# Kernel optimization log

Hardware: AMD Instinct MI355X
Metric: run time of the kernel (lower is better)

Reference implementation:

```python
import jax, jax.numpy as jnp
import numpy as np

N_HEADS = 16
D_HEAD = 64
THETA = 10000.0


def _rope_tables(S, dh, dtype):
    inv_freq = 1.0 / (THETA ** (jnp.arange(0, dh, 2, dtype=jnp.float32) / dh))  # [dh/2]
    ang = jnp.arange(S, dtype=jnp.float32)[:, None] * inv_freq[None, :]  # [S, dh/2]
    return jnp.cos(ang).astype(dtype), jnp.sin(ang).astype(dtype)


def _apply_rope(t, cos, sin):
    # t: [B,S,H,dh]; interleaved complex pairs (even=real, odd=imag)
    B, S, H, dh = t.shape
    tr = t.reshape(B, S, H, dh // 2, 2)
    a, b = tr[..., 0], tr[..., 1]
    c = cos[None, :, None, :]
    s = sin[None, :, None, :]
    ra = a * c - b * s
    rb = a * s + b * c
    return jnp.stack([ra, rb], axis=-1).reshape(B, S, H, dh)


def setup_inputs() -> dict:
    key = jax.random.key(0)
    ks = jax.random.split(key, 5)
    B, S, D = 2, 2048, 1024
    x = jax.random.normal(ks[0], (B, S, D), dtype=jnp.float32)
    scale = 1.0 / np.sqrt(D)
    wq = jax.random.normal(ks[1], (D, D), dtype=jnp.float32) * scale
    wk = jax.random.normal(ks[2], (D, D), dtype=jnp.float32) * scale
    wv = jax.random.normal(ks[3], (D, D), dtype=jnp.float32) * scale
    wo = jax.random.normal(ks[4], (D, D), dtype=jnp.float32) * scale
    return {"x": x, "wq": wq, "wk": wk, "wv": wv, "wo": wo}


def reference(x, wq, wk, wv, wo):
    B, S, D = x.shape
    H, dh = N_HEADS, D_HEAD
    q = (x @ wq).reshape(B, S, H, dh)
    k = (x @ wk).reshape(B, S, H, dh)
    v = (x @ wv).reshape(B, S, H, dh)
    cos, sin = _rope_tables(S, dh, x.dtype)
    q = _apply_rope(q, cos, sin)
    k = _apply_rope(k, cos, sin)
    # [B,H,S,S] scores
    scale = 1.0 / np.sqrt(dh).astype(np.float32)
    attn = jnp.einsum('bqhd,bkhd->bhqk', q, k) * scale
    causal = jnp.tril(jnp.ones((S, S), dtype=bool))[None, None]
    attn = jnp.where(causal, attn, -jnp.inf)
    probs = jax.nn.softmax(attn, axis=-1)
    head_out = jnp.einsum('bhqk,bkhd->bqhd', probs, v).reshape(B, S, D)
    return head_out @ wo
```

## Files before the change

### kernel.cpp

```cpp
#include <hip/hip_runtime.h>
#include <hip/hip_bf16.h>

#define S_LEN   2048
#define BATCH   2
#define NH      16
#define DH      64
#define DMODEL  1024
#define MTOT    (BATCH * S_LEN)

typedef __attribute__((ext_vector_type(4))) float f32x4;
typedef __attribute__((ext_vector_type(8))) short s16x8;
typedef __attribute__((ext_vector_type(4))) short s16x4;

#define MFMA_BF16(a, b, c) __builtin_amdgcn_mfma_f32_16x16x32_bf16((a), (b), (c), 0, 0, 0)

static __device__ __forceinline__ short f2bf(float f) {
    union { float f; unsigned u; } v; v.f = f;
    unsigned r = v.u + 0x7fffu + ((v.u >> 16) & 1u);
    return (short)(r >> 16);
}

static __device__ __forceinline__ unsigned cvtpk_bf16(float lo, float hi) {
    unsigned r;
    asm volatile("v_cvt_pk_bf16_f32 %0, %1, %2" : "=v"(r) : "v"(lo), "v"(hi));
    return r;
}

static __device__ __forceinline__ void gload_lds16(const void* g, void* l) {
    __builtin_amdgcn_global_load_lds(
        (const __attribute__((address_space(1))) void*)g,
        (__attribute__((address_space(3))) void*)l, 16, 0, 0);
}

#define VM_WAIT(N) asm volatile("s_waitcnt vmcnt(" #N ")" ::: "memory")

static __device__ __forceinline__ void barrier_sync() {
    asm volatile("" ::: "memory");
    __builtin_amdgcn_s_barrier();
    asm volatile("" ::: "memory");
}

__global__ __launch_bounds__(256) void prep_all(const float* __restrict__ wq,
                                                const float* __restrict__ wk,
                                                const float* __restrict__ wv,
                                                const float* __restrict__ wo,
                                                const float* __restrict__ x,
                                                short* __restrict__ wtb,
                                                short* __restrict__ xb,
                                                float* __restrict__ cosT,
                                                float* __restrict__ sinT) {
    const int t = threadIdx.x;
    if (blockIdx.z < 4) {
        const float* W = (blockIdx.z == 0) ? wq : (blockIdx.z == 1) ? wk
                       : (blockIdx.z == 2) ? wv : wo;
        short* out = wtb + (size_t)blockIdx.z * DMODEL * DMODEL;

        __shared__ short T[64][72];
        const int k0 = blockIdx.y * 64, n0 = blockIdx.x * 64;

        #pragma unroll
        for (int p = 0; p < 4; ++p) {
            const int kk = p * 16 + (t >> 4);
            const int nn = (t & 15) * 4;
            f32x4 v = *(const f32x4*)(W + (size_t)(k0 + kk) * DMODEL + n0 + nn);
            #pragma unroll
            for (int j = 0; j < 4; ++j) T[nn + j][kk] = f2bf(v[j]);
        }
        __syncthreads();
        #pragma unroll
        for (int p = 0; p < 4; ++p) {
            const int nn = p * 16 + (t >> 4);
            const int kk = (t & 15) * 4;
            *(s16x4*)(out + (size_t)(n0 + nn) * DMODEL + k0 + kk) = *(const s16x4*)&T[nn][kk];
        }
    } else {
        const int blk = blockIdx.y * 16 + blockIdx.x;
        #pragma unroll
        for (int jj = 0; jj < 8; ++jj) {
            const size_t i = ((size_t)jj * 65536 + blk * 256 + t) * 8;
            f32x4 a = *(const f32x4*)(x + i);
            f32x4 b = *(const f32x4*)(x + i + 4);
            s16x8 o;
            #pragma unroll
            for (int j = 0; j < 4; ++j) { o[j] = f2bf(a[j]); o[4 + j] = f2bf(b[j]); }
            *(s16x8*)(xb + i) = o;
        }
        const int idx = blk * 256 + t;
        const int s = idx >> 5, ii = idx & 31;
        const float inv = exp2f(-(float)ii * (13.287712379549449f / 32.0f));
        const float ang = (float)s * inv;
        cosT[idx] = cosf(ang);
        sinT[idx] = sinf(ang);
    }
}

__device__ __forceinline__ void gemm_tile(const short* __restrict__ A,
                                          const short* __restrict__ Bt,
                                          int m0, int n0, short* SM,
                                          f32x4 acc[4][4]) {
    const int tid  = threadIdx.x;
    const int lane = tid & 63;
    const int wv   = tid >> 6;
    const int wm   = (wv >> 1) * 64;
    const int wn   = (wv & 1) * 64;
    const int g = lane >> 4, c16 = lane & 15;

    short* Asb = SM;
    short* Bsb = SM + 12288;

    const int srow = tid >> 2;
    const int schk = (tid & 3) ^ ((tid >> 3) & 3);
    const short* ga0 = A  + (size_t)(m0 + srow)      * DMODEL + schk * 8;
    const short* ga1 = A  + (size_t)(m0 + 64 + srow) * DMODEL + schk * 8;
    const short* gb0 = Bt + (size_t)(n0 + srow)      * DMODEL + schk * 8;
    const short* gb1 = Bt + (size_t)(n0 + 64 + srow) * DMODEL + schk * 8;
    const int lw = wv * 512;

    #define STAGE_G(buf, ko) do { \
        gload_lds16(ga0 + (ko), Asb + (buf) * 4096 + lw); \
        gload_lds16(ga1 + (ko), Asb + (buf) * 4096 + 2048 + lw); \
        gload_lds16(gb0 + (ko), Bsb + (buf) * 4096 + lw); \
        gload_lds16(gb1 + (ko), Bsb + (buf) * 4096 + 2048 + lw); \
    } while (0)

    STAGE_G(0, 0);
    STAGE_G(1, 32);

    const int rlo = (g ^ ((c16 >> 1) & 3)) << 3;
    for (int ks = 0; ks < 32; ++ks) {
        if (ks < 31) { VM_WAIT(4); } else { VM_WAIT(0); }
        barrier_sync();
        if (ks + 2 < 32) STAGE_G((ks + 2) % 3, (ks + 2) * 32);
        const int cur = ks % 3;
        s16x8 af[4], bfr[4];
        #pragma unroll
        for (int i = 0; i < 4; ++i)
            af[i] = *(const s16x8*)&Asb[cur * 4096 + (wm + i * 16 + c16) * 32 + rlo];
        #pragma unroll
        for (int j = 0; j < 4; ++j)
            bfr[j] = *(const s16x8*)&Bsb[cur * 4096 + (wn + j * 16 + c16) * 32 + rlo];
        #pragma unroll
        for (int i = 0; i < 4; ++i)
            #pragma unroll
            for (int j = 0; j < 4; ++j)
                acc[i][j] = MFMA_BF16(af[i], bfr[j], acc[i][j]);
    }
    #undef STAGE_G
}

__global__ __launch_bounds__(256) void gemm_qkv(const short* __restrict__ xb,
                                                const short* __restrict__ wtb,
                                                short* __restrict__ Qo,
                                                short* __restrict__ Ko,
                                                short* __restrict__ Vt,
                                                const float* __restrict__ cosT,
                                                const float* __restrict__ sinT) {
    __shared__ __align__(16) short SM[24576];

    const int dd    = blockIdx.x + 24 * blockIdx.y;
    const int xcd   = dd & 7;
    const int local = dd >> 3;
    const int ty = (xcd & 3) * 8 + local / 12;
    const int tx = (xcd >> 2) * 12 + local % 12;
    const int m0 = ty * 128, n0 = tx * 128;
    const int z  = tx >> 3;

    f32x4 acc[4][4] = {};
    gemm_tile(xb, wtb, m0, n0, SM, acc);

    const int tid  = threadIdx.x;
    const int lane = tid & 63;
    const int wv   = tid >> 6;
    const int wm   = (wv >> 1) * 64, wn = (wv & 1) * 64;
    const int g = lane >> 4, c16 = lane & 15;
    const int hbase = (n0 & 1023) >> 6;

    barrier_sync();
    short (*RP)[136] = (short(*)[136])SM;

    if (z < 2) {
        short* outp = (z == 0) ? Qo : Ko;
        const float post = (z == 0) ? 0.18033688011112042f : 1.0f;
        #pragma unroll
        for (int j = 0; j < 4; ++j) {
            const int nl = wn + j * 16 + c16;
            const int d  = (n0 + nl) & 63;
            #pragma unroll
            for (int i = 0; i < 4; ++i) {
                #pragma unroll
                for (int r = 0; r < 4; ++r) {
                    const int ml = wm + i * 16 + g * 4 + r;
                    const int s  = (m0 + ml) & (S_LEN - 1);
                    float v = acc[i][j][r];
                    float vo = __shfl_xor(v, 1, 64);
                    float cs = cosT[s * 32 + (d >> 1)];
                    float sn = sinT[s * 32 + (d >> 1)];
                    float res = (d & 1) ? (vo * sn + v * cs) : (v * cs - vo * sn);
                    RP[ml][nl] = f2bf(res * post);
                }
            }
        }
        barrier_sync();
        #pragma unroll
        for (int pass = 0; pass < 8; ++pass) {
            const int row = pass * 32 + (tid >> 3);
            const int k   = tid & 7;
            const int hh = row >> 7, ss = row & 127;
            const int m = m0 + ss;
            const int s = m & (S_LEN - 1), b = m >> 11;
            short* dst = outp + (((size_t)b * NH + hbase + hh) * S_LEN + s) * DH + k * 8;
            *(s16x8*)dst = *(const s16x8*)&RP[ss][hh * 64 + k * 8];
        }
    } else {
        #pragma unroll
        for (int j = 0; j < 4; ++j) {
            const int nl = wn + j * 16 + c16;
            #pragma unroll
            for (int i = 0; i < 4; ++i) {
                const int mlb = wm + i * 16 + g * 4;
                s16x4 pk;
                #pragma unroll
                for (int r = 0; r < 4; ++r) pk[r] = f2bf(acc[i][j][r]);
                *(s16x4*)&RP[nl][mlb] = pk;
            }
        }
        barrier_sync();
        const int b = m0 >> 11, sr0 = m0 & (S_LEN - 1);
        #pragma unroll
        for (int pass = 0; pass < 8; ++pass) {
            const int row = pass * 16 + (tid >> 4);
            const int k   = tid & 15;
            const int h = hbase + (row >> 6), d = row & 63;
            short* dst = Vt + (((size_t)b * NH + h) * DH + d) * S_LEN + sr0 + k * 8;
            *(s16x8*)dst = *(const s16x8*)&RP[row][k * 8];
        }
    }
}

__global__ __launch_bounds__(256) void attn(const short* __restrict__ Q,
                                            const short* __restrict__ K,
                                            const short* __restrict__ Vt,
                                            short* __restrict__ O) {
    const int tid  = threadIdx.x;
    const int lane = tid & 63;
    const int w    = tid >> 6;
    const int g = lane >> 4, c16 = lane & 15;
    const int bid  = blockIdx.x + 16 * blockIdx.y;
    const int cxcd = bid & 7, jj = bid >> 3;
    const int bh   = (jj & 3) * 8 + cxcd;
    const int bx   = jj >> 2;
    const size_t base = (size_t)bh * S_LEN * DH;
    const short* Kb = K + base;
    const short* Vb = Vt + (size_t)bh * DH * S_LEN;
    const int b = bh >> 4, h = bh & 15;

    __shared__ __align__(16) short KL[3][4096];
    __shared__ __align__(16) short VL[3][4096];
    __shared__ __align__(16) short P2[4][16][72];

    const int kr = tid >> 3;
    const int kc = (tid & 7) ^ (kr & 7);
    const short* kg0 = Kb + (size_t)kr * DH + (kc << 3);
    const short* kg1 = Kb + (size_t)(32 + kr) * DH + (kc << 3);
    const short* vg0 = Vb + (size_t)kr * S_LEN + (kc << 3);
    const short* vg1 = Vb + (size_t)(32 + kr) * S_LEN + (kc << 3);
    const int lw = w * 512;
    const int kx = c16 & 7;

    #pragma unroll 1
    for (int half = 0; half < 2; ++half) {
        const int ci = half ? bx : 31 - bx;
        const int ntiles = ci + 1;
        const int wq0 = ci * 64 + w * 16;

        gload_lds16(kg0, &KL[0][lw]);
        gload_lds16(kg1, &KL[0][2048 + lw]);
        gload_lds16(vg0, &VL[0][lw]);
        gload_lds16(vg1, &VL[0][2048 + lw]);
        s16x8 bq0 = *(const s16x8*)(Q + base + (size_t)(wq0 + c16) * DH + g * 8);
        s16x8 bq1 = *(const s16x8*)(Q + base + (size_t)(wq0 + c16) * DH + 32 + g * 8);
        if (ntiles > 1) {
            gload_lds16(kg0 + (size_t)64 * DH, &KL[1][lw]);
            gload_lds16(kg1 + (size_t)64 * DH, &KL[1][2048 + lw]);
            gload_lds16(vg0 + 64, &VL[1][lw]);
            gload_lds16(vg1 + 64, &VL[1][2048 + lw]);
        }

        f32x4 o[4] = {};
        float lsum = 0.f;

        for (int tt = 0; tt < ntiles; ++tt) {
            if (tt + 1 < ntiles) { VM_WAIT(4); } else { VM_WAIT(0); }
            barrier_sync();
            if (tt + 2 < ntiles) {
                const int nb = (tt + 2) % 3;
                const size_t ko = (size_t)(tt + 2) * 64;
                gload_lds16(kg0 + ko * DH, &KL[nb][lw]);
                gload_lds16(kg1 + ko * DH, &KL[nb][2048 + lw]);
                gload_lds16(vg0 + ko,      &VL[nb][lw]);
                gload_lds16(vg1 + ko,      &VL[nb][2048 + lw]);
            }
            const int cur = tt % 3;

            f32x4 s[4];
            __builtin_amdgcn_s_setprio(1);
            #pragma unroll
            for (int cg = 0; cg < 4; ++cg) {
                const int krow = (cg * 16 + c16) * 64;
                s16x8 kf0 = *(const s16x8*)&KL[cur][krow + ((g ^ kx) << 3)];
                s16x8 kf1 = *(const s16x8*)&KL[cur][krow + (((4 + g) ^ kx) << 3)];
                f32x4 zz = {};
                zz = MFMA_BF16(kf0, bq0, zz);
                s[cg] = MFMA_BF16(kf1, bq1, zz);
            }
            __builtin_amdgcn_s_setprio(0);

            s16x8 vf[4][2];
            #pragma unroll
            for (int nt = 0; nt < 4; ++nt) {
                const int vr = (nt * 16 + c16) * 64;
                vf[nt][0] = *(const s16x8*)&VL[cur][vr + ((g ^ kx) << 3)];
                vf[nt][1] = *(const s16x8*)&VL[cur][vr + (((4 + g) ^ kx) << 3)];
            }

            const bool diag = (tt == ci);
            const int qrel = w * 16 + c16;
            #pragma unroll
            for (int cg = 0; cg < 4; ++cg) {
                float e[4];
                #pragma unroll
                for (int r = 0; r < 4; ++r) {
                    e[r] = exp2f(s[cg][r]);
                    if (diag && (cg * 16 + g * 4 + r > qrel)) e[r] = 0.f;
                }
                lsum += (e[0] + e[1]) + (e[2] + e[3]);
                uint2 pk;
                pk.x = cvtpk_bf16(e[0], e[1]);
                pk.y = cvtpk_bf16(e[2], e[3]);
                *(uint2*)&P2[w][c16][cg * 16 + g * 4] = pk;
            }
            asm volatile("s_waitcnt lgkmcnt(0)" ::: "memory");
            __builtin_amdgcn_sched_barrier(0);
            s16x8 ap0 = *(const s16x8*)&P2[w][c16][g * 8];
            s16x8 ap1 = *(const s16x8*)&P2[w][c16][32 + g * 8];

            __builtin_amdgcn_s_setprio(1);
            #pragma unroll
            for (int nt = 0; nt < 4; ++nt) {
                o[nt] = MFMA_BF16(ap0, vf[nt][0], o[nt]);
                o[nt] = MFMA_BF16(ap1, vf[nt][1], o[nt]);
            }
            __builtin_amdgcn_s_setprio(0);
        }

        float lt = lsum;
        lt += __shfl_xor(lt, 16, 64);
        lt += __shfl_xor(lt, 32, 64);
        #pragma unroll
        for (int r = 0; r < 4; ++r) {
            const float linv = 1.0f / __shfl(lt, g * 4 + r, 64);
            #pragma unroll
            for (int nt = 0; nt < 4; ++nt) {
                O[((size_t)(b * S_LEN + wq0 + g * 4 + r)) * DMODEL
                  + h * DH + nt * 16 + c16] = f2bf(o[nt][r] * linv);
            }
        }
    }
}

__global__ __launch_bounds__(256) void gemm_o(const short* __restrict__ Ob,
                                              const short* __restrict__ WoT,
                                              float* __restrict__ C) {
    __shared__ __align__(16) short SMl[24576];

    const int dd = blockIdx.x + 8 * blockIdx.y;
    const int ti = (dd & 7) * 32 + (dd >> 3);
    const int tx = ti & 7, ty = ti >> 3;
    const int m0 = ty * 128, n0 = tx * 128;

    f32x4 acc[4][4] = {};
    gemm_tile(Ob, WoT, m0, n0, SMl, acc);

    const int tid  = threadIdx.x;
    const int lane = tid & 63;
    const int wv   = tid >> 6;
    const int wm   = (wv >> 1) * 64, wn = (wv & 1) * 64;
    const int g = lane >> 4, c16 = lane & 15;

    #pragma unroll
    for (int i = 0; i < 4; ++i)
        #pragma unroll
        for (int j = 0; j < 4; ++j) {
            const int n = n0 + wn + j * 16 + c16;
            #pragma unroll
            for (int r = 0; r < 4; ++r) {
                const int m = m0 + wm + i * 16 + g * 4 + r;
                C[(size_t)m * DMODEL + n] = acc[i][j][r];
            }
        }
}

extern "C" void kernel_launch(void* const* d_in, const int* in_sizes, int n_in,
                              void* d_out, int out_size, void* d_ws, size_t ws_size,
                              hipStream_t stream) {
    const float* x  = (const float*)d_in[0];
    const float* wq = (const float*)d_in[1];
    const float* wk = (const float*)d_in[2];
    const float* wv = (const float*)d_in[3];
    const float* wo = (const float*)d_in[4];
    float* out = (float*)d_out;

    char* ws = (char*)d_ws;
    short* wtb  = (short*)ws;
    short* xb   = (short*)(ws + (8ull  << 20));
    float* cosT = (float*)(ws + (16ull << 20));
    float* sinT = (float*)(ws + (16ull << 20) + (256ull << 10));
    short* Qb   = (short*)(ws + (17ull << 20));
    short* Kb   = (short*)(ws + (25ull << 20));
    short* Vtb  = (short*)(ws + (33ull << 20));
    short* Ob   = (short*)(ws + (41ull << 20));

    prep_all<<<dim3(16, 16, 5), 256, 0, stream>>>(wq, wk, wv, wo, x,
                                                  wtb, xb, cosT, sinT);

    gemm_qkv<<<dim3(24, 32), 256, 0, stream>>>(xb, wtb, Qb, Kb, Vtb, cosT, sinT);
    attn    <<<dim3(16, 32), 256, 0, stream>>>(Qb, Kb, Vtb, Ob);
    gemm_o  <<<dim3(8, 32),  256, 0, stream>>>(Ob, wtb + 3ull * DMODEL * DMODEL, out);
}
```

Baseline: 110.0 us.

## Split attention blocks per query tile and use 128x64 tiles for output GEMM

The attention kernel drops the paired causal work balancing, where one block handled two query tiles, and now launches one block per (batch-head, query tile), for twice as many blocks. The K/V ring shrinks from triple to double buffering with a barrier at the end of each iteration. The output projection moves to a new 128x64 tile routine with more blocks, so more of the GPU's compute units get work. The cost is uneven per-block work under the causal mask, shallower prefetch in attention, and more redundant A-tile loads in the output GEMM.

```diff
diff --git a/kernel.cpp b/kernel.cpp
--- a/kernel.cpp
+++ b/kernel.cpp
@@ -148,6 +148,58 @@
     #undef STAGE_G
 }
 
+__device__ __forceinline__ void gemm_tile64(const short* __restrict__ A,
+                                            const short* __restrict__ Bt,
+                                            int m0, int n0, short* SM,
+                                            f32x4 acc[4][2]) {
+    const int tid  = threadIdx.x;
+    const int lane = tid & 63;
+    const int wv   = tid >> 6;
+    const int wm   = (wv >> 1) * 64;
+    const int wn   = (wv & 1) * 32;
+    const int g = lane >> 4, c16 = lane & 15;
+
+    short* Asb = SM;
+    short* Bsb = SM + 12288;
+
+    const int srow = tid >> 2;
+    const int schk = (tid & 3) ^ ((tid >> 3) & 3);
+    const short* ga0 = A  + (size_t)(m0 + srow)      * DMODEL + schk * 8;
+    const short* ga1 = A  + (size_t)(m0 + 64 + srow) * DMODEL + schk * 8;
+    const short* gb0 = Bt + (size_t)(n0 + srow)      * DMODEL + schk * 8;
+    const int lw = wv * 512;
+
+    #define SG64(buf, ko) do { \
+        gload_lds16(ga0 + (ko), Asb + (buf) * 4096 + lw); \
+        gload_lds16(ga1 + (ko), Asb + (buf) * 4096 + 2048 + lw); \
+        gload_lds16(gb0 + (ko), Bsb + (buf) * 2048 + lw); \
+    } while (0)
+
+    SG64(0, 0);
+    SG64(1, 32);
+
+    const int rlo = (g ^ ((c16 >> 1) & 3)) << 3;
+    for (int ks = 0; ks < 32; ++ks) {
+        if (ks < 31) { VM_WAIT(3); } else { VM_WAIT(0); }
+        barrier_sync();
+        if (ks + 2 < 32) SG64((ks + 2) % 3, (ks + 2) * 32);
+        const int cur = ks % 3;
+        s16x8 af[4], bfr[2];
+        #pragma unroll
+        for (int i = 0; i < 4; ++i)
+            af[i] = *(const s16x8*)&Asb[cur * 4096 + (wm + i * 16 + c16) * 32 + rlo];
+        #pragma unroll
+        for (int j = 0; j < 2; ++j)
+            bfr[j] = *(const s16x8*)&Bsb[cur * 2048 + (wn + j * 16 + c16) * 32 + rlo];
+        #pragma unroll
+        for (int i = 0; i < 4; ++i)
+            #pragma unroll
+            for (int j = 0; j < 2; ++j)
+                acc[i][j] = MFMA_BF16(af[i], bfr[j], acc[i][j]);
+    }
+    #undef SG64
+}
+
 __global__ __launch_bounds__(256) void gemm_qkv(const short* __restrict__ xb,
                                                 const short* __restrict__ wtb,
                                                 short* __restrict__ Qo,
@@ -245,17 +297,17 @@
     const int lane = tid & 63;
     const int w    = tid >> 6;
     const int g = lane >> 4, c16 = lane & 15;
-    const int bid  = blockIdx.x + 16 * blockIdx.y;
-    const int cxcd = bid & 7, jj = bid >> 3;
-    const int bh   = (jj & 3) * 8 + cxcd;
-    const int bx   = jj >> 2;
+    const int bh = blockIdx.x;
+    const int ci = 31 - blockIdx.y;
+    const int ntiles = ci + 1;
+    const int wq0 = ci * 64 + w * 16;
     const size_t base = (size_t)bh * S_LEN * DH;
     const short* Kb = K + base;
     const short* Vb = Vt + (size_t)bh * DH * S_LEN;
     const int b = bh >> 4, h = bh & 15;
 
-    __shared__ __align__(16) short KL[3][4096];
-    __shared__ __align__(16) short VL[3][4096];
+    __shared__ __align__(16) short KL[2][4096];
+    __shared__ __align__(16) short VL[2][4096];
     __shared__ __align__(16) short P2[4][16][72];
 
     const int kr = tid >> 3;
@@ -267,103 +319,93 @@
     const int lw = w * 512;
     const int kx = c16 & 7;
 
-    #pragma unroll 1
-    for (int half = 0; half < 2; ++half) {
-        const int ci = half ? bx : 31 - bx;
-        const int ntiles = ci + 1;
-        const int wq0 = ci * 64 + w * 16;
-
-        gload_lds16(kg0, &KL[0][lw]);
-        gload_lds16(kg1, &KL[0][2048 + lw]);
-        gload_lds16(vg0, &VL[0][lw]);
-        gload_lds16(vg1, &VL[0][2048 + lw]);
-        s16x8 bq0 = *(const s16x8*)(Q + base + (size_t)(wq0 + c16) * DH + g * 8);
-        s16x8 bq1 = *(const s16x8*)(Q + base + (size_t)(wq0 + c16) * DH + 32 + g * 8);
-        if (ntiles > 1) {
-            gload_lds16(kg0 + (size_t)64 * DH, &KL[1][lw]);
-            gload_lds16(kg1 + (size_t)64 * DH, &KL[1][2048 + lw]);
-            gload_lds16(vg0 + 64, &VL[1][lw]);
-            gload_lds16(vg1 + 64, &VL[1][2048 + lw]);
-        }
-
-        f32x4 o[4] = {};
-        float lsum = 0.f;
-
-        for (int tt = 0; tt < ntiles; ++tt) {
-            if (tt + 1 < ntiles) { VM_WAIT(4); } else { VM_WAIT(0); }
-            barrier_sync();
-            if (tt + 2 < ntiles) {
-                const int nb = (tt + 2) % 3;
-                const size_t ko = (size_t)(tt + 2) * 64;
-                gload_lds16(kg0 + ko * DH, &KL[nb][lw]);
-                gload_lds16(kg1 + ko * DH, &KL[nb][2048 + lw]);
-                gload_lds16(vg0 + ko,      &VL[nb][lw]);
-                gload_lds16(vg1 + ko,      &VL[nb][2048 + lw]);
+    gload_lds16(kg0, &KL[0][lw]);
+    gload_lds16(kg1, &KL[0][2048 + lw]);
+    gload_lds16(vg0, &VL[0][lw]);
+    gload_lds16(vg1, &VL[0][2048 + lw]);
+    s16x8 bq0 = *(const s16x8*)(Q + base + (size_t)(wq0 + c16) * DH + g * 8);
+    s16x8 bq1 = *(const s16x8*)(Q + base + (size_t)(wq0 + c16) * DH + 32 + g * 8);
+    VM_WAIT(0);
+    barrier_sync();
+
+    f32x4 o[4] = {};
+    float lsum = 0.f;
+
+    for (int tt = 0; tt < ntiles; ++tt) {
+        const int cur = tt & 1;
+        const bool more = (tt + 1 < ntiles);
+        if (more) {
+            const size_t ko = (size_t)(tt + 1) * 64;
+            gload_lds16(kg0 + ko * DH, &KL[cur ^ 1][lw]);
+            gload_lds16(kg1 + ko * DH, &KL[cur ^ 1][2048 + lw]);
+            gload_lds16(vg0 + ko,      &VL[cur ^ 1][lw]);
+            gload_lds16(vg1 + ko,      &VL[cur ^ 1][2048 + lw]);
+        }
+
+        f32x4 s[4];
+        __builtin_amdgcn_s_setprio(1);
+        #pragma unroll
+        for (int cg = 0; cg < 4; ++cg) {
+            const int krow = (cg * 16 + c16) * 64;
+            s16x8 kf0 = *(const s16x8*)&KL[cur][krow + ((g ^ kx) << 3)];
+            s16x8 kf1 = *(const s16x8*)&KL[cur][krow + (((4 + g) ^ kx) << 3)];
+            f32x4 zz = {};
+            zz = MFMA_BF16(kf0, bq0, zz);
+            s[cg] = MFMA_BF16(kf1, bq1, zz);
+        }
+        __builtin_amdgcn_s_setprio(0);
+
+        s16x8 vf[4][2];
+        #pragma unroll
+        for (int nt = 0; nt < 4; ++nt) {
+            const int vr = (nt * 16 + c16) * 64;
+            vf[nt][0] = *(const s16x8*)&VL[cur][vr + ((g ^ kx) << 3)];
+            vf[nt][1] = *(const s16x8*)&VL[cur][vr + (((4 + g) ^ kx) << 3)];
+        }
+
+        const bool diag = (tt == ci);
+        const int qrel = w * 16 + c16;
+        #pragma unroll
+        for (int cg = 0; cg < 4; ++cg) {
+            float e[4];
+            #pragma unroll
+            for (int r = 0; r < 4; ++r) {
+                e[r] = exp2f(s[cg][r]);
+                if (diag && (cg * 16 + g * 4 + r > qrel)) e[r] = 0.f;
             }
-            const int cur = tt % 3;
-
-            f32x4 s[4];
-            __builtin_amdgcn_s_setprio(1);
-            #pragma unroll
-            for (int cg = 0; cg < 4; ++cg) {
-                const int krow = (cg * 16 + c16) * 64;
-                s16x8 kf0 = *(const s16x8*)&KL[cur][krow + ((g ^ kx) << 3)];
-                s16x8 kf1 = *(const s16x8*)&KL[cur][krow + (((4 + g) ^ kx) << 3)];
-                f32x4 zz = {};
-                zz = MFMA_BF16(kf0, bq0, zz);
-                s[cg] = MFMA_BF16(kf1, bq1, zz);
-            }
-            __builtin_amdgcn_s_setprio(0);
-
-            s16x8 vf[4][2];
-            #pragma unroll
-            for (int nt = 0; nt < 4; ++nt) {
-                const int vr = (nt * 16 + c16) * 64;
-                vf[nt][0] = *(const s16x8*)&VL[cur][vr + ((g ^ kx) << 3)];
-                vf[nt][1] = *(const s16x8*)&VL[cur][vr + (((4 + g) ^ kx) << 3)];
-            }
-
-            const bool diag = (tt == ci);
-            const int qrel = w * 16 + c16;
-            #pragma unroll
-            for (int cg = 0; cg < 4; ++cg) {
-                float e[4];
-                #pragma unroll
-                for (int r = 0; r < 4; ++r) {
-                    e[r] = exp2f(s[cg][r]);
-                    if (diag && (cg * 16 + g * 4 + r > qrel)) e[r] = 0.f;
-                }
-                lsum += (e[0] + e[1]) + (e[2] + e[3]);
-                uint2 pk;
-                pk.x = cvtpk_bf16(e[0], e[1]);
-                pk.y = cvtpk_bf16(e[2], e[3]);
-                *(uint2*)&P2[w][c16][cg * 16 + g * 4] = pk;
-            }
-            asm volatile("s_waitcnt lgkmcnt(0)" ::: "memory");
-            __builtin_amdgcn_sched_barrier(0);
-            s16x8 ap0 = *(const s16x8*)&P2[w][c16][g * 8];
-            s16x8 ap1 = *(const s16x8*)&P2[w][c16][32 + g * 8];
-
-            __builtin_amdgcn_s_setprio(1);
-            #pragma unroll
-            for (int nt = 0; nt < 4; ++nt) {
-                o[nt] = MFMA_BF16(ap0, vf[nt][0], o[nt]);
-                o[nt] = MFMA_BF16(ap1, vf[nt][1], o[nt]);
-            }
-            __builtin_amdgcn_s_setprio(0);
-        }
-
-        float lt = lsum;
-        lt += __shfl_xor(lt, 16, 64);
-        lt += __shfl_xor(lt, 32, 64);
-        #pragma unroll
-        for (int r = 0; r < 4; ++r) {
-            const float linv = 1.0f / __shfl(lt, g * 4 + r, 64);
-            #pragma unroll
-            for (int nt = 0; nt < 4; ++nt) {
-                O[((size_t)(b * S_LEN + wq0 + g * 4 + r)) * DMODEL
-                  + h * DH + nt * 16 + c16] = f2bf(o[nt][r] * linv);
-            }
+            lsum += (e[0] + e[1]) + (e[2] + e[3]);
+            uint2 pk;
+            pk.x = cvtpk_bf16(e[0], e[1]);
+            pk.y = cvtpk_bf16(e[2], e[3]);
+            *(uint2*)&P2[w][c16][cg * 16 + g * 4] = pk;
+        }
+        asm volatile("s_waitcnt lgkmcnt(0)" ::: "memory");
+        __builtin_amdgcn_sched_barrier(0);
+        s16x8 ap0 = *(const s16x8*)&P2[w][c16][g * 8];
+        s16x8 ap1 = *(const s16x8*)&P2[w][c16][32 + g * 8];
+
+        __builtin_amdgcn_s_setprio(1);
+        #pragma unroll
+        for (int nt = 0; nt < 4; ++nt) {
+            o[nt] = MFMA_BF16(ap0, vf[nt][0], o[nt]);
+            o[nt] = MFMA_BF16(ap1, vf[nt][1], o[nt]);
+        }
+        __builtin_amdgcn_s_setprio(0);
+
+        if (more) { VM_WAIT(0); }
+        barrier_sync();
+    }
+
+    float lt = lsum;
+    lt += __shfl_xor(lt, 16, 64);
+    lt += __shfl_xor(lt, 32, 64);
+    #pragma unroll
+    for (int r = 0; r < 4; ++r) {
+        const float linv = 1.0f / __shfl(lt, g * 4 + r, 64);
+        #pragma unroll
+        for (int nt = 0; nt < 4; ++nt) {
+            O[((size_t)(b * S_LEN + wq0 + g * 4 + r)) * DMODEL
+              + h * DH + nt * 16 + c16] = f2bf(o[nt][r] * linv);
         }
     }
 }
@@ -371,26 +413,26 @@
 __global__ __launch_bounds__(256) void gemm_o(const short* __restrict__ Ob,
                                               const short* __restrict__ WoT,
                                               float* __restrict__ C) {
-    __shared__ __align__(16) short SMl[24576];
-
-    const int dd = blockIdx.x + 8 * blockIdx.y;
-    const int ti = (dd & 7) * 32 + (dd >> 3);
-    const int tx = ti & 7, ty = ti >> 3;
-    const int m0 = ty * 128, n0 = tx * 128;
-
-    f32x4 acc[4][4] = {};
-    gemm_tile(Ob, WoT, m0, n0, SMl, acc);
+    __shared__ __align__(16) short SMl[18432];
+
+    const int dd = blockIdx.x + 16 * blockIdx.y;
+    const int ti = (dd & 7) * 64 + (dd >> 3);
+    const int tx = ti & 15, ty = ti >> 4;
+    const int m0 = ty * 128, n0 = tx * 64;
+
+    f32x4 acc[4][2] = {};
+    gemm_tile64(Ob, WoT, m0, n0, SMl, acc);
 
     const int tid  = threadIdx.x;
     const int lane = tid & 63;
     const int wv   = tid >> 6;
-    const int wm   = (wv >> 1) * 64, wn = (wv & 1) * 64;
+    const int wm   = (wv >> 1) * 64, wn = (wv & 1) * 32;
     const int g = lane >> 4, c16 = lane & 15;
 
     #pragma unroll
     for (int i = 0; i < 4; ++i)
         #pragma unroll
-        for (int j = 0; j < 4; ++j) {
+        for (int j = 0; j < 2; ++j) {
             const int n = n0 + wn + j * 16 + c16;
             #pragma unroll
             for (int r = 0; r < 4; ++r) {
@@ -424,6 +466,6 @@
                                                   wtb, xb, cosT, sinT);
 
     gemm_qkv<<<dim3(24, 32), 256, 0, stream>>>(xb, wtb, Qb, Kb, Vtb, cosT, sinT);
-    attn    <<<dim3(16, 32), 256, 0, stream>>>(Qb, Kb, Vtb, Ob);
-    gemm_o  <<<dim3(8, 32),  256, 0, stream>>>(Ob, wtb + 3ull * DMODEL * DMODEL, out);
-}
+    attn    <<<dim3(32, 32), 256, 0, stream>>>(Qb, Kb, Vtb, Ob);
+    gemm_o  <<<dim3(16, 32), 256, 0, stream>>>(Ob, wtb + 3ull * DMODEL * DMODEL, out);
+}
```

Measured after the change: 109.2 us. About the same (-0.7%).
